# Kernel optimization log

Measured on AMD Instinct MI355X. Metric: run time of the kernel, lower is better.

The kernel has to match this reference:

```python
import jax, jax.numpy as jnp
import numpy as np

N, D = 262144, 64
C, K, NSPLITS = 16, 4 + 12, 4  # K=16 codewords per codebook (2**NSPLITS)
K = 16
M = 16


def setup_inputs() -> dict:
    key = jax.random.key(0)
    k1, k2, k3, k4, k5 = jax.random.split(key, 5)
    A = jax.random.normal(k1, (N, D), dtype=jnp.float32)
    B = jax.random.normal(k2, (M, D), dtype=jnp.float32)
    prototypes = jax.random.normal(k3, (C, K, D), dtype=jnp.float32)
    split_dims = jax.random.randint(k4, (C, NSPLITS), 0, D, dtype=jnp.int32)
    # level i of the binary tree uses 2**i thresholds; pad to 2**(NSPLITS-1)=8
    split_vals = jax.random.normal(k5, (C, NSPLITS, 2 ** (NSPLITS - 1)), dtype=jnp.float32)
    return {"A": A, "B": B, "prototypes": prototypes,
            "split_dims": split_dims, "split_vals": split_vals}


def _encode(A, split_dims, split_vals):
    # Vectorized maddness_encode / apply_hash_function over all C codebooks.
    n = A.shape[0]
    c = split_dims.shape[0]
    nsplits = split_dims.shape[1]
    c_idx = jnp.arange(c)[None, :]                      # [1, C]
    group_ids = jnp.zeros((n, c), dtype=jnp.int32)      # [N, C]
    for i in range(nsplits):                            # fixed tiny loop (4 levels)
        x = A[:, split_dims[:, i]]                      # [N, C] gather of split dim
        vals_i = split_vals[:, i, :]                    # [C, 8]
        v = vals_i[c_idx, group_ids]                    # [N, C] per-group threshold
        group_ids = group_ids * 2 + (x > v).astype(jnp.int32)
    return group_ids                                    # [N, C] in [0, K)


def reference(A, B, prototypes, split_dims, split_vals):
    # 1) encode A rows: binary-tree hash per codebook -> codeword ids
    A_enc = _encode(A, split_dims, split_vals)          # [N, C] int32
    # 2) LUTs: luts[m, c, k] = <B[m], prototypes[c, k]>  (maddness_lut per row)
    luts = jnp.einsum('md,ckd->ckm', B, prototypes)     # [C, K, M]
    # 3) LUT-based accumulate (quantize_lut=False path): sum over codebooks
    c_idx = jnp.arange(luts.shape[0])[None, :]          # [1, C]
    g = luts[c_idx, A_enc]                              # [N, C, M] gathered LUT entries
    out = g.sum(axis=1).T                               # [M, N]
    return out
```

## Files before the change

### kernel.cpp

```cpp
#include <hip/hip_runtime.h>


#define NROWS 262144
#define DDIM  64
#define CNUM  16
#define KPROT 16
#define MOUT  16
#define TPB   128
#define TILE  128
#define TILES_PER_BLOCK 4
#define NBLOCKS 512
#define LSTRIDE 20
#define RSTRIDE 65

__global__ __launch_bounds__(TPB) void maddness_kernel(
    const float* __restrict__ A,
    const float* __restrict__ B,
    const float* __restrict__ P,
    const int*   __restrict__ sd,
    const float* __restrict__ sv,
    float* __restrict__ out)
{
    __shared__ __align__(16) float lut_s[CNUM * KPROT * LSTRIDE];
    __shared__ __align__(16) float sv_s[CNUM * 32];
    __shared__ __align__(16) float rows_s[TILE * RSTRIDE];

    const int t = threadIdx.x;

    {
        const int m = t & 15;
        float4 brow[16];
        const float4* B4 = (const float4*)(B + m * DDIM);
        #pragma unroll
        for (int j = 0; j < 16; ++j) brow[j] = B4[j];

        #pragma unroll
        for (int j = 0; j < 32; ++j) {
            int o = j * TPB + t;
            int c = o >> 8;
            int k = (o >> 4) & 15;
            const float4* P4 = (const float4*)(P + (c * KPROT + k) * DDIM);
            float dot = 0.f;
            #pragma unroll
            for (int q = 0; q < 16; ++q) {
                float4 p = P4[q];
                dot += p.x * brow[q].x + p.y * brow[q].y
                     + p.z * brow[q].z + p.w * brow[q].w;
            }
            lut_s[(c * KPROT + k) * LSTRIDE + m] = dot;
        }
        ((float4*)sv_s)[t] = ((const float4*)sv)[t];
    }

    const float4* A4 = (const float4*)A;
    float4 R[16];
    {
        long base = (long)blockIdx.x * (TILE * DDIM / 4);
        #pragma unroll
        for (int j = 0; j < 16; ++j) R[j] = A4[base + j * TPB + t];
    }

    for (int s = 0; s < TILES_PER_BLOCK; ++s) {
        const int tile = blockIdx.x + s * NBLOCKS;

        __syncthreads();

        #pragma unroll
        for (int j = 0; j < 16; ++j) {
            int e   = j * TPB + t;
            int row = e >> 4;
            int col = (e & 15) * 4;
            float* dst = &rows_s[row * RSTRIDE + col];
            float4 v = R[j];
            dst[0] = v.x; dst[1] = v.y; dst[2] = v.z; dst[3] = v.w;
        }
        if (s + 1 < TILES_PER_BLOCK) {
            long base = (long)(tile + NBLOCKS) * (TILE * DDIM / 4);
            #pragma unroll
            for (int j = 0; j < 16; ++j) R[j] = A4[base + j * TPB + t];
        }

        __syncthreads();

        float acc[MOUT];
        #pragma unroll
        for (int m = 0; m < MOUT; ++m) acc[m] = 0.f;

        const float* rrow = &rows_s[t * RSTRIDE];

        #pragma unroll
        for (int c = 0; c < CNUM; ++c) {
            const int   sd0 = sd[c * 4 + 0], sd1 = sd[c * 4 + 1];
            const int   sd2 = sd[c * 4 + 2], sd3 = sd[c * 4 + 3];
            const float v0  = sv[c * 32 + 0];
            const float v1a = sv[c * 32 + 8];
            const float v1b = sv[c * 32 + 9];

            int g = (rrow[sd0] > v0) ? 1 : 0;
            float v1 = g ? v1b : v1a;
            g = (g << 1) | ((rrow[sd1] > v1) ? 1 : 0);
            float v2 = sv_s[c * 32 + 16 + g];
            g = (g << 1) | ((rrow[sd2] > v2) ? 1 : 0);
            float v3 = sv_s[c * 32 + 24 + g];
            g = (g << 1) | ((rrow[sd3] > v3) ? 1 : 0);

            const float4* lp = (const float4*)&lut_s[(c * KPROT + g) * LSTRIDE];
            float4 p0 = lp[0], p1 = lp[1], p2 = lp[2], p3 = lp[3];
            acc[0]  += p0.x; acc[1]  += p0.y; acc[2]  += p0.z; acc[3]  += p0.w;
            acc[4]  += p1.x; acc[5]  += p1.y; acc[6]  += p1.z; acc[7]  += p1.w;
            acc[8]  += p2.x; acc[9]  += p2.y; acc[10] += p2.z; acc[11] += p2.w;
            acc[12] += p3.x; acc[13] += p3.y; acc[14] += p3.z; acc[15] += p3.w;
        }

        const int n = tile * TILE + t;
        #pragma unroll
        for (int m = 0; m < MOUT; ++m)
            out[(long)m * NROWS + n] = acc[m];
    }
}

extern "C" void kernel_launch(void* const* d_in, const int* in_sizes, int n_in,
                              void* d_out, int out_size, void* d_ws, size_t ws_size,
                              hipStream_t stream) {
    const float* A  = (const float*)d_in[0];
    const float* B  = (const float*)d_in[1];
    const float* P  = (const float*)d_in[2];
    const int*   sd = (const int*)d_in[3];
    const float* sv = (const float*)d_in[4];
    float* out = (float*)d_out;

    maddness_kernel<<<dim3(NBLOCKS), dim3(TPB), 0, stream>>>(A, B, P, sd, sv, out);
}
```

Baseline: 125.2 us.

## Split LUT build into separate kernel, use fp16 LUT and packed half accumulation

LUT construction moves out of the main kernel into a small pre-kernel that writes fp16 LUT entries to workspace, so each block no longer recomputes the full LUT. The main kernel now processes one tile per block (2048 blocks), stores A column-major in shared memory, selects thresholds from registers instead of shared memory, and accumulates the gathered LUT rows as packed half8 vectors split into even and odd codebook sums. This cuts redundant per-block LUT work and shared-memory traffic. In exchange it adds a second launch and loses accuracy from fp16 LUT values and fp16 accumulation.

```diff
diff --git a/kernel.cpp b/kernel.cpp
--- a/kernel.cpp
+++ b/kernel.cpp
@@ -1,121 +1,115 @@
 #include <hip/hip_runtime.h>
+#include <hip/hip_fp16.h>
 
 
 #define NROWS 262144
 #define DDIM  64
-#define CNUM  16
-#define KPROT 16
-#define MOUT  16
 #define TPB   128
-#define TILE  128
-#define TILES_PER_BLOCK 4
-#define NBLOCKS 512
-#define LSTRIDE 20
-#define RSTRIDE 65
+#define NBLK  2048
+#define RSTR  129
+#define LSTR  24
 
-__global__ __launch_bounds__(TPB) void maddness_kernel(
-    const float* __restrict__ A,
+typedef __attribute__((ext_vector_type(8))) _Float16 half8;
+typedef __attribute__((ext_vector_type(4))) unsigned int u32x4;
+
+__global__ __launch_bounds__(256) void lut_build(
     const float* __restrict__ B,
     const float* __restrict__ P,
+    _Float16* __restrict__ lutw)
+{
+    int o = blockIdx.x * 256 + threadIdx.x;
+    int m  = o & 15;
+    int ck = o >> 4;
+    const float4* Bp = (const float4*)(B + m * DDIM);
+    const float4* Pp = (const float4*)(P + ck * DDIM);
+    float dot = 0.f;
+    #pragma unroll
+    for (int q = 0; q < 16; ++q) {
+        float4 b = Bp[q], p = Pp[q];
+        dot += b.x * p.x + b.y * p.y + b.z * p.z + b.w * p.w;
+    }
+    lutw[o] = (_Float16)dot;
+}
+
+__global__ __launch_bounds__(TPB, 2) void maddness_main(
+    const float* __restrict__ A,
     const int*   __restrict__ sd,
     const float* __restrict__ sv,
+    const _Float16* __restrict__ lutw,
     float* __restrict__ out)
 {
-    __shared__ __align__(16) float lut_s[CNUM * KPROT * LSTRIDE];
-    __shared__ __align__(16) float sv_s[CNUM * 32];
-    __shared__ __align__(16) float rows_s[TILE * RSTRIDE];
+    __shared__ float rows_s[DDIM * RSTR];
+    __shared__ __align__(16) _Float16 lut_s[256 * LSTR];
 
     const int t = threadIdx.x;
 
-    {
-        const int m = t & 15;
-        float4 brow[16];
-        const float4* B4 = (const float4*)(B + m * DDIM);
-        #pragma unroll
-        for (int j = 0; j < 16; ++j) brow[j] = B4[j];
-
-        #pragma unroll
-        for (int j = 0; j < 32; ++j) {
-            int o = j * TPB + t;
-            int c = o >> 8;
-            int k = (o >> 4) & 15;
-            const float4* P4 = (const float4*)(P + (c * KPROT + k) * DDIM);
-            float dot = 0.f;
-            #pragma unroll
-            for (int q = 0; q < 16; ++q) {
-                float4 p = P4[q];
-                dot += p.x * brow[q].x + p.y * brow[q].y
-                     + p.z * brow[q].z + p.w * brow[q].w;
-            }
-            lut_s[(c * KPROT + k) * LSTRIDE + m] = dot;
-        }
-        ((float4*)sv_s)[t] = ((const float4*)sv)[t];
+    #pragma unroll
+    for (int i = 0; i < 2; ++i) {
+        int e = t + i * TPB;
+        const u32x4* src = (const u32x4*)(lutw + e * 16);
+        u32x4 q0 = src[0], q1 = src[1];
+        *(u32x4*)(lut_s + e * LSTR)     = q0;
+        *(u32x4*)(lut_s + e * LSTR + 8) = q1;
     }
 
     const float4* A4 = (const float4*)A;
+    long base = (long)blockIdx.x * (TPB * DDIM / 4);
     float4 R[16];
-    {
-        long base = (long)blockIdx.x * (TILE * DDIM / 4);
-        #pragma unroll
-        for (int j = 0; j < 16; ++j) R[j] = A4[base + j * TPB + t];
+    #pragma unroll
+    for (int j = 0; j < 16; ++j) R[j] = A4[base + j * TPB + t];
+    #pragma unroll
+    for (int j = 0; j < 16; ++j) {
+        int f    = j * TPB + t;
+        int row  = f >> 4;
+        int colq = (f & 15) * 4;
+        rows_s[(colq + 0) * RSTR + row] = R[j].x;
+        rows_s[(colq + 1) * RSTR + row] = R[j].y;
+        rows_s[(colq + 2) * RSTR + row] = R[j].z;
+        rows_s[(colq + 3) * RSTR + row] = R[j].w;
     }
 
-    for (int s = 0; s < TILES_PER_BLOCK; ++s) {
-        const int tile = blockIdx.x + s * NBLOCKS;
+    __syncthreads();
 
-        __syncthreads();
+    half8 aE0 = {0,0,0,0,0,0,0,0}, aE1 = {0,0,0,0,0,0,0,0};
+    half8 aO0 = {0,0,0,0,0,0,0,0}, aO1 = {0,0,0,0,0,0,0,0};
 
-        #pragma unroll
-        for (int j = 0; j < 16; ++j) {
-            int e   = j * TPB + t;
-            int row = e >> 4;
-            int col = (e & 15) * 4;
-            float* dst = &rows_s[row * RSTRIDE + col];
-            float4 v = R[j];
-            dst[0] = v.x; dst[1] = v.y; dst[2] = v.z; dst[3] = v.w;
-        }
-        if (s + 1 < TILES_PER_BLOCK) {
-            long base = (long)(tile + NBLOCKS) * (TILE * DDIM / 4);
-            #pragma unroll
-            for (int j = 0; j < 16; ++j) R[j] = A4[base + j * TPB + t];
-        }
+    #pragma unroll
+    for (int c = 0; c < 16; ++c) {
+        const int sd0 = sd[c*4+0], sd1 = sd[c*4+1], sd2 = sd[c*4+2], sd3 = sd[c*4+3];
+        float x0 = rows_s[sd0 * RSTR + t];
+        float x1 = rows_s[sd1 * RSTR + t];
+        float x2 = rows_s[sd2 * RSTR + t];
+        float x3 = rows_s[sd3 * RSTR + t];
+        const float* svc = sv + c * 32;
 
-        __syncthreads();
+        int g = (x0 > svc[0]) ? 1 : 0;
+        float v1 = g ? svc[9] : svc[8];
+        g = (g << 1) | ((x1 > v1) ? 1 : 0);
+        float ta = (g & 1) ? svc[17] : svc[16];
+        float tb = (g & 1) ? svc[19] : svc[18];
+        float v2 = (g & 2) ? tb : ta;
+        g = (g << 1) | ((x2 > v2) ? 1 : 0);
+        float u0 = (g & 1) ? svc[25] : svc[24];
+        float u1 = (g & 1) ? svc[27] : svc[26];
+        float u2 = (g & 1) ? svc[29] : svc[28];
+        float u3 = (g & 1) ? svc[31] : svc[30];
+        float w0 = (g & 2) ? u1 : u0;
+        float w1 = (g & 2) ? u3 : u2;
+        float v3 = (g & 4) ? w1 : w0;
+        g = (g << 1) | ((x3 > v3) ? 1 : 0);
 
-        float acc[MOUT];
-        #pragma unroll
-        for (int m = 0; m < MOUT; ++m) acc[m] = 0.f;
+        const _Float16* lp = lut_s + (c * 16 + g) * LSTR;
+        half8 l0 = *(const half8*)(lp);
+        half8 l1 = *(const half8*)(lp + 8);
+        if (c & 1) { aO0 += l0; aO1 += l1; }
+        else       { aE0 += l0; aE1 += l1; }
+    }
 
-        const float* rrow = &rows_s[t * RSTRIDE];
-
-        #pragma unroll
-        for (int c = 0; c < CNUM; ++c) {
-            const int   sd0 = sd[c * 4 + 0], sd1 = sd[c * 4 + 1];
-            const int   sd2 = sd[c * 4 + 2], sd3 = sd[c * 4 + 3];
-            const float v0  = sv[c * 32 + 0];
-            const float v1a = sv[c * 32 + 8];
-            const float v1b = sv[c * 32 + 9];
-
-            int g = (rrow[sd0] > v0) ? 1 : 0;
-            float v1 = g ? v1b : v1a;
-            g = (g << 1) | ((rrow[sd1] > v1) ? 1 : 0);
-            float v2 = sv_s[c * 32 + 16 + g];
-            g = (g << 1) | ((rrow[sd2] > v2) ? 1 : 0);
-            float v3 = sv_s[c * 32 + 24 + g];
-            g = (g << 1) | ((rrow[sd3] > v3) ? 1 : 0);
-
-            const float4* lp = (const float4*)&lut_s[(c * KPROT + g) * LSTRIDE];
-            float4 p0 = lp[0], p1 = lp[1], p2 = lp[2], p3 = lp[3];
-            acc[0]  += p0.x; acc[1]  += p0.y; acc[2]  += p0.z; acc[3]  += p0.w;
-            acc[4]  += p1.x; acc[5]  += p1.y; acc[6]  += p1.z; acc[7]  += p1.w;
-            acc[8]  += p2.x; acc[9]  += p2.y; acc[10] += p2.z; acc[11] += p2.w;
-            acc[12] += p3.x; acc[13] += p3.y; acc[14] += p3.z; acc[15] += p3.w;
-        }
-
-        const int n = tile * TILE + t;
-        #pragma unroll
-        for (int m = 0; m < MOUT; ++m)
-            out[(long)m * NROWS + n] = acc[m];
+    const int n = blockIdx.x * TPB + t;
+    #pragma unroll
+    for (int m = 0; m < 8; ++m) {
+        out[(long)m       * NROWS + n] = (float)aE0[m] + (float)aO0[m];
+        out[(long)(m + 8) * NROWS + n] = (float)aE1[m] + (float)aO1[m];
     }
 }
 
@@ -128,6 +122,8 @@
     const int*   sd = (const int*)d_in[3];
     const float* sv = (const float*)d_in[4];
     float* out = (float*)d_out;
+    _Float16* lutw = (_Float16*)d_ws;
 
-    maddness_kernel<<<dim3(NBLOCKS), dim3(TPB), 0, stream>>>(A, B, P, sd, sv, out);
+    lut_build<<<dim3(16), dim3(256), 0, stream>>>(B, P, lutw);
+    maddness_main<<<dim3(NBLK), dim3(TPB), 0, stream>>>(A, sd, sv, lutw, out);
 }
```

New measurement: 124.2 us. No clear change (-0.8%).
